# Kernel optimization log

Hardware: AMD Instinct MI355X
Metric: run time of the kernel (lower is better)

The kernel has to match this reference:

```python
import jax, jax.numpy as jnp
import numpy as np

B, T, IN, H = 1024, 128, 5, 100  # batch, seq_len, input_size, hidden_size


def setup_inputs() -> dict:
    key = jax.random.key(0)
    ks = jax.random.split(key, 20)
    bound = 1.0 / np.sqrt(H)  # PyTorch LSTM init: U(-1/sqrt(H), 1/sqrt(H))

    def u(k, shape):
        return jax.random.uniform(k, shape, jnp.float32, -bound, bound)

    inp = {"x": jax.random.normal(ks[0], (B, T, IN), jnp.float32)}
    i = 1
    for layer, din in [(0, IN), (1, 2 * H)]:
        for d in ("f", "b"):
            inp[f"w_ih_l{layer}{d}"] = u(ks[i], (4 * H, din)); i += 1
            inp[f"w_hh_l{layer}{d}"] = u(ks[i], (4 * H, H)); i += 1
            inp[f"b_ih_l{layer}{d}"] = u(ks[i], (4 * H,)); i += 1
            inp[f"b_hh_l{layer}{d}"] = u(ks[i], (4 * H,)); i += 1
    inp["fc_w"] = u(ks[17], (3, 2 * H))
    inp["fc_b"] = u(ks[18], (3,))
    return inp


def _run_dir(x, w_ih, w_hh, b_ih, b_hh, reverse):
    """One LSTM direction. x: [B,T,D] -> hidden seq [B,T,H]. PyTorch gate order i,f,g,o."""
    xT = jnp.swapaxes(x, 0, 1)  # [T,B,D]
    # precompute input contribution for all timesteps: [T,B,4H]
    xg = jnp.einsum('tbd,gd->tbg', xT, w_ih) + b_ih + b_hh

    def step(carry, g_in):
        h, c = carry
        g = g_in + h @ w_hh.T  # [B,4H]
        i, f, gg, o = jnp.split(g, 4, axis=-1)
        c = jax.nn.sigmoid(f) * c + jax.nn.sigmoid(i) * jnp.tanh(gg)
        h = jax.nn.sigmoid(o) * jnp.tanh(c)
        return (h, c), h

    b = x.shape[0]
    init = (jnp.zeros((b, H), x.dtype), jnp.zeros((b, H), x.dtype))
    _, hs = jax.lax.scan(step, init, xg, reverse=reverse)  # hs[t] aligned with time t
    return jnp.swapaxes(hs, 0, 1)  # [B,T,H]


def reference(x,
              w_ih_l0f, w_hh_l0f, b_ih_l0f, b_hh_l0f,
              w_ih_l0b, w_hh_l0b, b_ih_l0b, b_hh_l0b,
              w_ih_l1f, w_hh_l1f, b_ih_l1f, b_hh_l1f,
              w_ih_l1b, w_hh_l1b, b_ih_l1b, b_hh_l1b,
              fc_w, fc_b):
    # Layer 0 (bidirectional): [B,T,2H]
    h0 = jnp.concatenate([
        _run_dir(x, w_ih_l0f, w_hh_l0f, b_ih_l0f, b_hh_l0f, False),
        _run_dir(x, w_ih_l0b, w_hh_l0b, b_ih_l0b, b_hh_l0b, True),
    ], axis=-1)
    # (inter-layer dropout p=0.2 is identity in eval mode)
    # Layer 1 (bidirectional): [B,T,2H]
    h1 = jnp.concatenate([
        _run_dir(h0, w_ih_l1f, w_hh_l1f, b_ih_l1f, b_hh_l1f, False),
        _run_dir(h0, w_ih_l1b, w_hh_l1b, b_ih_l1b, b_hh_l1b, True),
    ], axis=-1)
    last = h1[:, -1, :]  # [B,2H]
    # (dropout p=0.5 is identity in eval mode)
    logits = last @ fc_w.T + fc_b  # [B,3]
    return jax.nn.softmax(logits, axis=1)
```

## Files before the change

kernel.cpp:

```cpp
#include <hip/hip_runtime.h>
#include <hip/hip_fp16.h>


typedef __attribute__((ext_vector_type(8))) short bf16x8;
typedef __attribute__((ext_vector_type(4))) float f32x4;

constexpr int Bsz = 1024, Tt = 128, IN_ = 5, H = 100, G = 400, D1 = 200;
constexpr int NP = 512;
constexpr int NT = 25;
constexpr int MB = 8;
constexpr int MB1 = 4;

__device__ __forceinline__ float sigm(float x)   { return 1.f / (1.f + __expf(-x)); }
__device__ __forceinline__ float tanhf_(float x) { return 1.f - 2.f / (__expf(2.f * x) + 1.f); }
__device__ __forceinline__ unsigned short f2bf(float f) {
  unsigned u = __float_as_uint(f);
  u += 0x7fff + ((u >> 16) & 1);
  return (unsigned short)(u >> 16);
}
__device__ __forceinline__ float partner8(float v) {
  return __uint_as_float(
      (unsigned)__builtin_amdgcn_ds_swizzle((int)__float_as_uint(v), 0x17));
}
__device__ __forceinline__ float partner4(float v) {
  return __uint_as_float(
      (unsigned)__builtin_amdgcn_ds_swizzle((int)__float_as_uint(v), 0x13));
}

__device__ __forceinline__ void pack_body(
    const float* wA, int KA, const float* wB, int KB, int kbo,
    const float* b1, const float* b2, int bias_k,
    unsigned short* dst, int Kg, int idx) {
  if (idx >= Kg * NP * 8) return;
  int jj = idx & 7, rest = idx >> 3;
  int np_ = rest % NP, g = rest / NP;
  int j = np_ >> 2, gate = np_ & 3;
  int k = g * 8 + jj;
  float v = 0.f;
  if (j < H) {
    int n = gate * H + j;
    if (k < KA) v = wA[n * KA + k];
    else if (KB > 0 && k >= kbo && k < kbo + KB) v = wB[n * KB + (k - kbo)];
    else if (k == bias_k) v = b1[n] + b2[n];
  }
  dst[idx] = f2bf(v);
}

__global__ void pack_all(
    const float* __restrict__ w_hh_l0f, const float* __restrict__ w_ih_l0f,
    const float* __restrict__ b_ih_l0f, const float* __restrict__ b_hh_l0f,
    const float* __restrict__ w_hh_l0b, const float* __restrict__ w_ih_l0b,
    const float* __restrict__ b_ih_l0b, const float* __restrict__ b_hh_l0b,
    const float* __restrict__ w_hh_l1f, const float* __restrict__ b_ih_l1f,
    const float* __restrict__ b_hh_l1f,
    const float* __restrict__ w_ih_l1f, const float* __restrict__ w_ih_l1b,
    const float* __restrict__ b_ih_l1b, const float* __restrict__ b_hh_l1b,
    unsigned short* __restrict__ pk0f, unsigned short* __restrict__ pk0b,
    unsigned short* __restrict__ pkhh, unsigned short* __restrict__ pkxg,
    unsigned short* __restrict__ pk1b) {
  int idx = blockIdx.x * 256 + threadIdx.x;
  switch (blockIdx.y) {
    case 0: pack_body(w_hh_l0f, 100, w_ih_l0f, 5, 100, b_ih_l0f, b_hh_l0f, 105, pk0f, 16, idx); break;
    case 1: pack_body(w_hh_l0b, 100, w_ih_l0b, 5, 100, b_ih_l0b, b_hh_l0b, 105, pk0b, 16, idx); break;
    case 2: pack_body(w_hh_l1f, 100, nullptr, 0, 0, b_ih_l1f, b_hh_l1f, -1, pkhh, 16, idx); break;
    case 3: pack_body(w_ih_l1f, 200, nullptr, 0, 0, b_ih_l1f, b_hh_l1f, 200, pkxg, 28, idx); break;
    default: pack_body(w_ih_l1b, 200, nullptr, 0, 0, b_ih_l1b, b_hh_l1b, 200, pk1b, 28, idx);
  }
}

__global__ __launch_bounds__(1024, 1) void lstm_l0(
    const float* __restrict__ x,
    const unsigned short* __restrict__ pk_f, const unsigned short* __restrict__ pk_b,
    unsigned short* __restrict__ h0fT, unsigned short* __restrict__ h0bT) {
  __shared__ __align__(16) short A_s[2][16][16][8];

  const int tid = threadIdx.x;
  const int lane = tid & 63, w = tid >> 6;
  const int q = lane >> 4, l16 = lane & 15;
  const int b0 = blockIdx.x * MB;
  const int dir = blockIdx.y;
  const unsigned short* pk = dir ? pk_b : pk_f;
  unsigned short* hT = dir ? h0bT : h0fT;

  for (int i = tid; i < 2 * 16 * 16 * 8; i += 1024) ((short*)A_s)[i] = 0;

  const int mtA = w, mtB = w + 16;
  const bool bvalid = (mtB < NT);
  bf16x8 wfA[4], wfB[4];
#pragma unroll
  for (int kt = 0; kt < 4; ++kt) {
    wfA[kt] = *(const bf16x8*)(pk + ((size_t)(kt * 4 + q) * NP + mtA * 16 + l16) * 8);
    wfB[kt] = *(const bf16x8*)(pk + ((size_t)(kt * 4 + q) * NP + mtB * 16 + l16) * 8);
  }
  float c = 0.f;
  const bool up = (l16 >= 8);
  const int mm = l16 & 7;
  const int j = (up ? mtB : mtA) * 4 + q;
  const bool valid = up ? bvalid : true;
  const int xm = tid / IN_, xe = tid - xm * IN_;
  const int sm = tid / 25, sj = (tid - (tid / 25) * 25) * 4;
  const float* xp = x + ((size_t)(b0 + xm) * Tt + (dir ? Tt - 2 : 1)) * IN_ + xe;
  const int xstride = dir ? -IN_ : IN_;
  unsigned short* hp =
      hT + ((size_t)(dir ? Tt - 1 : 0) * Bsz + b0 + sm) * H + sj;
  const int hstride = dir ? -(Bsz * H) : (Bsz * H);
  __syncthreads();
  if (tid < 16) {
    A_s[0][13][tid][1] = (short)f2bf(1.f);
    A_s[1][13][tid][1] = (short)f2bf(1.f);
  }
  if (tid < MB * IN_) {
    int t0 = dir ? (Tt - 1) : 0;
    int k = 100 + xe;
    A_s[0][k >> 3][xm][k & 7] =
        (short)f2bf(x[((size_t)(b0 + xm) * Tt + t0) * IN_ + xe]);
  }
  __syncthreads();

  int p = 0;
  for (int step = 0; step < Tt; ++step) {
    if (step > 0 && tid < 200) {
      uint2 hv = *(const uint2*)&A_s[p][sj >> 3][sm][sj & 7];
      *(uint2*)hp = hv;
      hp += hstride;
    }
    float xn = 0.f;
    const bool do_x = (tid < MB * IN_) && (step < Tt - 1);
    if (do_x) { xn = *xp; xp += xstride; }
    bf16x8 hfrag[4];
#pragma unroll
    for (int kt = 0; kt < 4; ++kt) hfrag[kt] = *(const bf16x8*)A_s[p][kt * 4 + q][l16];
    f32x4 accA = (f32x4){0.f, 0.f, 0.f, 0.f};
    f32x4 accB = (f32x4){0.f, 0.f, 0.f, 0.f};
#pragma unroll
    for (int kt = 0; kt < 4; ++kt)
      accA = __builtin_amdgcn_mfma_f32_16x16x32_bf16(wfA[kt], hfrag[kt], accA, 0, 0, 0);
    if (bvalid) {
#pragma unroll
      for (int kt = 0; kt < 4; ++kt)
        accB = __builtin_amdgcn_mfma_f32_16x16x32_bf16(wfB[kt], hfrag[kt], accB, 0, 0, 0);
    }
    float pb0 = partner8(accB[0]), pb1 = partner8(accB[1]);
    float pb2 = partner8(accB[2]), pb3 = partner8(accB[3]);
    float g0 = up ? pb0 : accA[0];
    float g1 = up ? pb1 : accA[1];
    float g2 = up ? pb2 : accA[2];
    float g3 = up ? pb3 : accA[3];
    float cc = sigm(g1) * c + sigm(g0) * tanhf_(g2);
    c = cc;
    float h = sigm(g3) * tanhf_(cc);
    if (valid) A_s[1 - p][j >> 3][mm][j & 7] = (short)f2bf(h);
    if (do_x) {
      int k = 100 + xe;
      A_s[1 - p][k >> 3][xm][k & 7] = (short)f2bf(xn);
    }
    __syncthreads();
    p ^= 1;
  }
  if (tid < 200) *(uint2*)hp = *(const uint2*)&A_s[p][sj >> 3][sm][sj & 7];
}

__global__ __launch_bounds__(1024, 1) void gemm_xg(
    const unsigned short* __restrict__ h0fT, const unsigned short* __restrict__ h0bT,
    const unsigned short* __restrict__ pkw, __half* __restrict__ xg) {
  __shared__ __align__(16) short B_s[28][64][8];
  const int tid = threadIdx.x;
  const int lane = tid & 63, w = tid >> 6;
  const int q = lane >> 4, l16 = lane & 15;
  const int r0 = blockIdx.x * 64;
  const size_t base = (size_t)r0 * H;

  for (int i = tid; i < 3 * 64 * 8; i += 1024) {
    int jj = i & 7, gl = i >> 9;
    ((short*)&B_s[25][0][0])[i] = (short)((gl == 0 && jj == 0) ? f2bf(1.f) : 0);
  }
  for (int idx = tid; idx < 1600; idx += 1024) {
    int m = idx / 25, j0 = (idx - (idx / 25) * 25) * 4;
    *(uint2*)&B_s[j0 >> 3][m][j0 & 7] = *(const uint2*)(h0fT + base + m * H + j0);
    int k = 100 + j0;
    *(uint2*)&B_s[k >> 3][m][k & 7] = *(const uint2*)(h0bT + base + m * H + j0);
  }

  const int mtA = w, mtB = w + 16;
  const bool bvalid = (mtB < NT);
  bf16x8 wfA[7], wfB[7];
#pragma unroll
  for (int kt = 0; kt < 7; ++kt) {
    wfA[kt] = *(const bf16x8*)(pkw + ((size_t)(kt * 4 + q) * NP + mtA * 16 + l16) * 8);
    wfB[kt] = *(const bf16x8*)(pkw + ((size_t)(kt * 4 + q) * NP + mtB * 16 + l16) * 8);
  }
  const int jA = mtA * 4 + q, jB = mtB * 4 + q;
  __syncthreads();

#pragma unroll
  for (int rg = 0; rg < 4; ++rg) {
    f32x4 accA = (f32x4){0.f, 0.f, 0.f, 0.f};
    f32x4 accB = (f32x4){0.f, 0.f, 0.f, 0.f};
#pragma unroll
    for (int kt = 0; kt < 7; ++kt) {
      bf16x8 hf = *(const bf16x8*)B_s[kt * 4 + q][rg * 16 + l16];
      accA = __builtin_amdgcn_mfma_f32_16x16x32_bf16(wfA[kt], hf, accA, 0, 0, 0);
      if (bvalid)
        accB = __builtin_amdgcn_mfma_f32_16x16x32_bf16(wfB[kt], hf, accB, 0, 0, 0);
    }
    const size_t row = (size_t)(r0 + rg * 16 + l16);
    {
      __half2 h01 = __floats2half2_rn(accA[0], accA[1]);
      __half2 h23 = __floats2half2_rn(accA[2], accA[3]);
      uint2 st; *(__half2*)&st.x = h01; *(__half2*)&st.y = h23;
      *(uint2*)(xg + row * G + 4 * jA) = st;
    }
    if (bvalid) {
      __half2 h01 = __floats2half2_rn(accB[0], accB[1]);
      __half2 h23 = __floats2half2_rn(accB[2], accB[3]);
      uint2 st; *(__half2*)&st.x = h01; *(__half2*)&st.y = h23;
      *(uint2*)(xg + row * G + 4 * jB) = st;
    }
  }
}

__global__ __launch_bounds__(1024, 1) void lstm_l1(
    const unsigned short* __restrict__ h0fT, const unsigned short* __restrict__ h0bT,
    const unsigned short* __restrict__ pk_hh, const unsigned short* __restrict__ pk1b,
    const __half* __restrict__ xg,
    const float* __restrict__ fc_w, const float* __restrict__ fc_b,
    float* __restrict__ out) {
  __shared__ __align__(16) short A_s[2][16][16][8];
  __shared__ __align__(16) short A2_s[28][16][8];
  __shared__ float hf_s[MB1][H];
  __shared__ float hb_s[MB1][H];
  __shared__ float fcw_s[3 * D1];
  __shared__ float fcb_s[3];
  __shared__ float logit_s[MB1][3];

  const int tid = threadIdx.x;
  const int lane = tid & 63, w = tid >> 6;
  const int q = lane >> 4, l16 = lane & 15;
  const int b0 = blockIdx.x * MB1;
  const uint2* xg2 = (const uint2*)xg;

  for (int i = tid; i < 2 * 16 * 16 * 8; i += 1024) ((short*)A_s)[i] = 0;
  for (int i = tid; i < 25 * 16 * 8; i += 1024) ((short*)A2_s)[i] = 0;
  for (int i = tid; i < 3 * 16 * 8; i += 1024) {
    int jj = i & 7, gl = i >> 7;
    ((short*)&A2_s[25][0][0])[i] = (short)((gl == 0 && jj == 0) ? f2bf(1.f) : 0);
  }
  for (int i = tid; i < 3 * D1; i += 1024) fcw_s[i] = fc_w[i];
  if (tid < 3) fcb_s[tid] = fc_b[tid];

  const bool busy = (w < 7);
  const int m = l16 & 3, g16 = l16 >> 2;
  const int myMt = w * 4 + g16;
  const int jme = myMt * 4 + q;
  const bool evalid = busy && (myMt < NT);
  int mts[4]; bool tv[4];
  bf16x8 wf[4][4];
  if (busy) {
#pragma unroll
    for (int i = 0; i < 4; ++i) {
      int mt = w * 4 + i; mts[i] = mt; tv[i] = (mt < NT);
#pragma unroll
      for (int kt = 0; kt < 4; ++kt)
        wf[i][kt] = *(const bf16x8*)(pk_hh + ((size_t)(kt * 4 + q) * NP + mt * 16 + l16) * 8);
    }
  }
  float c = 0.f;
  const uint2* xgp = xg2 + (size_t)(b0 + m) * 100 + jme;
  uint2 xgCur = {0, 0};
  if (busy) { xgCur = *xgp; xgp += Bsz * 100; }
  __syncthreads();

  int p = 0;
  for (int t = 0; t < Tt; ++t) {
    if (busy) {
      uint2 xgNxt = xgCur;
      if (t < Tt - 1) { xgNxt = *xgp; xgp += Bsz * 100; }
      bf16x8 hfrag[4];
#pragma unroll
      for (int kt = 0; kt < 4; ++kt) hfrag[kt] = *(const bf16x8*)A_s[p][kt * 4 + q][l16];
      f32x4 acc[4];
#pragma unroll
      for (int i = 0; i < 4; ++i) {
        acc[i] = (f32x4){0.f, 0.f, 0.f, 0.f};
        if (!tv[i]) continue;
#pragma unroll
        for (int kt = 0; kt < 4; ++kt)
          acc[i] = __builtin_amdgcn_mfma_f32_16x16x32_bf16(wf[i][kt], hfrag[kt], acc[i], 0, 0, 0);
      }
      float2 x01 = __half22float2(*(const __half2*)&xgCur.x);
      float2 x23 = __half22float2(*(const __half2*)&xgCur.y);
      float xr[4] = {x01.x, x01.y, x23.x, x23.y};
      float gr[4];
#pragma unroll
      for (int r = 0; r < 4; ++r) {
        float v0 = partner4(acc[0][r]);
        float v1 = partner4(acc[1][r]);
        float v2 = partner4(acc[2][r]);
        float v3 = partner4(acc[3][r]);
        float lo = (g16 & 1) ? v1 : v0;
        float hi = (g16 & 1) ? v3 : v2;
        gr[r] = ((g16 & 2) ? hi : lo) + xr[r];
      }
      float cc = sigm(gr[1]) * c + sigm(gr[0]) * tanhf_(gr[2]);
      c = cc;
      float h = sigm(gr[3]) * tanhf_(cc);
      if (evalid) {
        A_s[1 - p][jme >> 3][m][jme & 7] = (short)f2bf(h);
        if (t == Tt - 1) hf_s[m][jme] = h;
      }
      xgCur = xgNxt;
    }
    __syncthreads();
    p ^= 1;
  }

  {
    const size_t base = ((size_t)(Tt - 1) * Bsz + b0) * H;
    if (tid < 100) {
      int m2 = tid / 25, j0 = (tid - (tid / 25) * 25) * 4;
      *(uint2*)&A2_s[j0 >> 3][m2][j0 & 7] = *(const uint2*)(h0fT + base + m2 * H + j0);
      int k = 100 + j0;
      *(uint2*)&A2_s[k >> 3][m2][k & 7] = *(const uint2*)(h0bT + base + m2 * H + j0);
    }
  }
  __syncthreads();
  if (busy) {
    f32x4 acc[4];
#pragma unroll
    for (int i = 0; i < 4; ++i) acc[i] = (f32x4){0.f, 0.f, 0.f, 0.f};
#pragma unroll
    for (int kt = 0; kt < 7; ++kt) {
      bf16x8 hf = *(const bf16x8*)A2_s[kt * 4 + q][l16];
#pragma unroll
      for (int i = 0; i < 4; ++i) {
        if (!tv[i]) continue;
        bf16x8 wfb = *(const bf16x8*)(pk1b + ((size_t)(kt * 4 + q) * NP + mts[i] * 16 + l16) * 8);
        acc[i] = __builtin_amdgcn_mfma_f32_16x16x32_bf16(wfb, hf, acc[i], 0, 0, 0);
      }
    }
    float gr[4];
#pragma unroll
    for (int r = 0; r < 4; ++r) {
      float v0 = partner4(acc[0][r]);
      float v1 = partner4(acc[1][r]);
      float v2 = partner4(acc[2][r]);
      float v3 = partner4(acc[3][r]);
      float lo = (g16 & 1) ? v1 : v0;
      float hi = (g16 & 1) ? v3 : v2;
      gr[r] = (g16 & 2) ? hi : lo;
    }
    float cc = sigm(gr[0]) * tanhf_(gr[2]);
    if (evalid) hb_s[m][jme] = sigm(gr[3]) * tanhf_(cc);
  }
  __syncthreads();

  if (tid < MB1 * 3) {
    int mr = tid / 3, cls = tid - mr * 3;
    float s = fcb_s[cls];
    for (int jj = 0; jj < H; ++jj) s += fcw_s[cls * D1 + jj] * hf_s[mr][jj];
    for (int jj = 0; jj < H; ++jj) s += fcw_s[cls * D1 + H + jj] * hb_s[mr][jj];
    logit_s[mr][cls] = s;
  }
  __syncthreads();
  if (tid < MB1) {
    float a = logit_s[tid][0], b = logit_s[tid][1], cc = logit_s[tid][2];
    float mx = fmaxf(a, fmaxf(b, cc));
    float e0 = __expf(a - mx), e1 = __expf(b - mx), e2 = __expf(cc - mx);
    float inv = 1.f / (e0 + e1 + e2);
    out[(b0 + tid) * 3 + 0] = e0 * inv;
    out[(b0 + tid) * 3 + 1] = e1 * inv;
    out[(b0 + tid) * 3 + 2] = e2 * inv;
  }
}

extern "C" void kernel_launch(void* const* d_in, const int* in_sizes, int n_in,
                              void* d_out, int out_size, void* d_ws, size_t ws_size,
                              hipStream_t stream) {
  const float* x        = (const float*)d_in[0];
  const float* w_ih_l0f = (const float*)d_in[1];
  const float* w_hh_l0f = (const float*)d_in[2];
  const float* b_ih_l0f = (const float*)d_in[3];
  const float* b_hh_l0f = (const float*)d_in[4];
  const float* w_ih_l0b = (const float*)d_in[5];
  const float* w_hh_l0b = (const float*)d_in[6];
  const float* b_ih_l0b = (const float*)d_in[7];
  const float* b_hh_l0b = (const float*)d_in[8];
  const float* w_ih_l1f = (const float*)d_in[9];
  const float* w_hh_l1f = (const float*)d_in[10];
  const float* b_ih_l1f = (const float*)d_in[11];
  const float* b_hh_l1f = (const float*)d_in[12];
  const float* w_ih_l1b = (const float*)d_in[13];
  const float* b_ih_l1b = (const float*)d_in[15];
  const float* b_hh_l1b = (const float*)d_in[16];
  const float* fc_w     = (const float*)d_in[17];
  const float* fc_b     = (const float*)d_in[18];

  unsigned short* h0fT = (unsigned short*)d_ws;
  unsigned short* h0bT = h0fT + (size_t)Tt * Bsz * H;
  __half* xgT          = (__half*)(h0bT + (size_t)Tt * Bsz * H);
  unsigned short* pk0f = (unsigned short*)(xgT + (size_t)Tt * Bsz * G);
  unsigned short* pk0b = pk0f + 16 * NP * 8;
  unsigned short* pkhh = pk0b + 16 * NP * 8;
  unsigned short* pkxg = pkhh + 16 * NP * 8;
  unsigned short* pk1b = pkxg + 28 * NP * 8;

  pack_all<<<dim3(448, 5), 256, 0, stream>>>(
      w_hh_l0f, w_ih_l0f, b_ih_l0f, b_hh_l0f,
      w_hh_l0b, w_ih_l0b, b_ih_l0b, b_hh_l0b,
      w_hh_l1f, b_ih_l1f, b_hh_l1f,
      w_ih_l1f, w_ih_l1b, b_ih_l1b, b_hh_l1b,
      pk0f, pk0b, pkhh, pkxg, pk1b);

  lstm_l0<<<dim3(Bsz / MB, 2), 1024, 0, stream>>>(x, pk0f, pk0b, h0fT, h0bT);
  gemm_xg<<<(Bsz * Tt) / 64, 1024, 0, stream>>>(h0fT, h0bT, pkxg, xgT);
  lstm_l1<<<Bsz / MB1, 1024, 0, stream>>>(h0fT, h0bT, pkhh, pk1b, xgT,
                                          fc_w, fc_b, (float*)d_out);
}
```

Measured before the change: 383.4 us.

## Halve per-block batch in both LSTM kernels and use 512-thread blocks with more occupancy

Cuts the batch rows per block (8 to 4 in layer 0, 4 to 2 in layer 1) and shrinks blocks to 512 threads with launch bounds allowing 4 blocks per CU. Layer 0 is rebuilt so each of 7 busy waves handles four gate tiles, with a partner4 swizzle replacing the old two-tile split. Layer 1 switches to a partner2 swizzle for the narrower batch. The aim is more blocks in flight so the serial recurrence latency is hidden across more CUs. In exchange, more MFMA work is spent on padded batch columns and each block reloads the weights.

```diff
diff --git a/kernel.cpp b/kernel.cpp
--- a/kernel.cpp
+++ b/kernel.cpp
@@ -8,8 +8,8 @@
 constexpr int Bsz = 1024, Tt = 128, IN_ = 5, H = 100, G = 400, D1 = 200;
 constexpr int NP = 512;
 constexpr int NT = 25;
-constexpr int MB = 8;
-constexpr int MB1 = 4;
+constexpr int MB = 4;
+constexpr int MB1 = 2;
 
 __device__ __forceinline__ float sigm(float x)   { return 1.f / (1.f + __expf(-x)); }
 __device__ __forceinline__ float tanhf_(float x) { return 1.f - 2.f / (__expf(2.f * x) + 1.f); }
@@ -18,13 +18,13 @@
   u += 0x7fff + ((u >> 16) & 1);
   return (unsigned short)(u >> 16);
 }
-__device__ __forceinline__ float partner8(float v) {
-  return __uint_as_float(
-      (unsigned)__builtin_amdgcn_ds_swizzle((int)__float_as_uint(v), 0x17));
-}
 __device__ __forceinline__ float partner4(float v) {
   return __uint_as_float(
       (unsigned)__builtin_amdgcn_ds_swizzle((int)__float_as_uint(v), 0x13));
+}
+__device__ __forceinline__ float partner2(float v) {
+  return __uint_as_float(
+      (unsigned)__builtin_amdgcn_ds_swizzle((int)__float_as_uint(v), 0x11));
 }
 
 __device__ __forceinline__ void pack_body(
@@ -68,7 +68,7 @@
   }
 }
 
-__global__ __launch_bounds__(1024, 1) void lstm_l0(
+__global__ __launch_bounds__(512, 4) void lstm_l0(
     const float* __restrict__ x,
     const unsigned short* __restrict__ pk_f, const unsigned short* __restrict__ pk_b,
     unsigned short* __restrict__ h0fT, unsigned short* __restrict__ h0bT) {
@@ -82,22 +82,29 @@
   const unsigned short* pk = dir ? pk_b : pk_f;
   unsigned short* hT = dir ? h0bT : h0fT;
 
-  for (int i = tid; i < 2 * 16 * 16 * 8; i += 1024) ((short*)A_s)[i] = 0;
-
-  const int mtA = w, mtB = w + 16;
-  const bool bvalid = (mtB < NT);
-  bf16x8 wfA[4], wfB[4];
-#pragma unroll
-  for (int kt = 0; kt < 4; ++kt) {
-    wfA[kt] = *(const bf16x8*)(pk + ((size_t)(kt * 4 + q) * NP + mtA * 16 + l16) * 8);
-    wfB[kt] = *(const bf16x8*)(pk + ((size_t)(kt * 4 + q) * NP + mtB * 16 + l16) * 8);
+  for (int i = tid; i < 2 * 16 * 16 * 8; i += 512) ((short*)A_s)[i] = 0;
+
+  const bool busy = (w < 7);
+  const int m = l16 & 3, g16 = l16 >> 2;
+  const int myMt = w * 4 + g16;
+  const int jme = myMt * 4 + q;
+  const bool evalid = busy && (myMt < NT);
+  bool tv[4];
+  bf16x8 wf[4][4];
+  if (busy) {
+#pragma unroll
+    for (int i = 0; i < 4; ++i) {
+      int mt = w * 4 + i; tv[i] = (mt < NT);
+#pragma unroll
+      for (int kt = 0; kt < 4; ++kt)
+        wf[i][kt] = *(const bf16x8*)(pk + ((size_t)(kt * 4 + q) * NP + mt * 16 + l16) * 8);
+    }
   }
   float c = 0.f;
-  const bool up = (l16 >= 8);
-  const int mm = l16 & 7;
-  const int j = (up ? mtB : mtA) * 4 + q;
-  const bool valid = up ? bvalid : true;
-  const int xm = tid / IN_, xe = tid - xm * IN_;
+  const int xt = tid - 448;
+  const bool xl = (xt >= 0 && xt < MB * IN_);
+  const int xm = xl ? xt / IN_ : 0;
+  const int xe = xl ? xt - xm * IN_ : 0;
   const int sm = tid / 25, sj = (tid - (tid / 25) * 25) * 4;
   const float* xp = x + ((size_t)(b0 + xm) * Tt + (dir ? Tt - 2 : 1)) * IN_ + xe;
   const int xstride = dir ? -IN_ : IN_;
@@ -111,45 +118,51 @@
   }
   if (tid < MB * IN_) {
     int t0 = dir ? (Tt - 1) : 0;
-    int k = 100 + xe;
-    A_s[0][k >> 3][xm][k & 7] =
-        (short)f2bf(x[((size_t)(b0 + xm) * Tt + t0) * IN_ + xe]);
+    int m0 = tid / IN_, e0 = tid - m0 * IN_;
+    int k = 100 + e0;
+    A_s[0][k >> 3][m0][k & 7] =
+        (short)f2bf(x[((size_t)(b0 + m0) * Tt + t0) * IN_ + e0]);
   }
   __syncthreads();
 
   int p = 0;
   for (int step = 0; step < Tt; ++step) {
-    if (step > 0 && tid < 200) {
-      uint2 hv = *(const uint2*)&A_s[p][sj >> 3][sm][sj & 7];
-      *(uint2*)hp = hv;
+    if (step > 0 && tid < 100) {
+      *(uint2*)hp = *(const uint2*)&A_s[p][sj >> 3][sm][sj & 7];
       hp += hstride;
     }
     float xn = 0.f;
-    const bool do_x = (tid < MB * IN_) && (step < Tt - 1);
+    const bool do_x = xl && (step < Tt - 1);
     if (do_x) { xn = *xp; xp += xstride; }
-    bf16x8 hfrag[4];
-#pragma unroll
-    for (int kt = 0; kt < 4; ++kt) hfrag[kt] = *(const bf16x8*)A_s[p][kt * 4 + q][l16];
-    f32x4 accA = (f32x4){0.f, 0.f, 0.f, 0.f};
-    f32x4 accB = (f32x4){0.f, 0.f, 0.f, 0.f};
-#pragma unroll
-    for (int kt = 0; kt < 4; ++kt)
-      accA = __builtin_amdgcn_mfma_f32_16x16x32_bf16(wfA[kt], hfrag[kt], accA, 0, 0, 0);
-    if (bvalid) {
-#pragma unroll
-      for (int kt = 0; kt < 4; ++kt)
-        accB = __builtin_amdgcn_mfma_f32_16x16x32_bf16(wfB[kt], hfrag[kt], accB, 0, 0, 0);
-    }
-    float pb0 = partner8(accB[0]), pb1 = partner8(accB[1]);
-    float pb2 = partner8(accB[2]), pb3 = partner8(accB[3]);
-    float g0 = up ? pb0 : accA[0];
-    float g1 = up ? pb1 : accA[1];
-    float g2 = up ? pb2 : accA[2];
-    float g3 = up ? pb3 : accA[3];
-    float cc = sigm(g1) * c + sigm(g0) * tanhf_(g2);
-    c = cc;
-    float h = sigm(g3) * tanhf_(cc);
-    if (valid) A_s[1 - p][j >> 3][mm][j & 7] = (short)f2bf(h);
+    if (busy) {
+      bf16x8 hfrag[4];
+#pragma unroll
+      for (int kt = 0; kt < 4; ++kt) hfrag[kt] = *(const bf16x8*)A_s[p][kt * 4 + q][l16];
+      f32x4 acc[4];
+#pragma unroll
+      for (int i = 0; i < 4; ++i) {
+        acc[i] = (f32x4){0.f, 0.f, 0.f, 0.f};
+        if (!tv[i]) continue;
+#pragma unroll
+        for (int kt = 0; kt < 4; ++kt)
+          acc[i] = __builtin_amdgcn_mfma_f32_16x16x32_bf16(wf[i][kt], hfrag[kt], acc[i], 0, 0, 0);
+      }
+      float gr[4];
+#pragma unroll
+      for (int r = 0; r < 4; ++r) {
+        float v0 = partner4(acc[0][r]);
+        float v1 = partner4(acc[1][r]);
+        float v2 = partner4(acc[2][r]);
+        float v3 = partner4(acc[3][r]);
+        float lo = (g16 & 1) ? v1 : v0;
+        float hi = (g16 & 1) ? v3 : v2;
+        gr[r] = (g16 & 2) ? hi : lo;
+      }
+      float cc = sigm(gr[1]) * c + sigm(gr[0]) * tanhf_(gr[2]);
+      c = cc;
+      float h = sigm(gr[3]) * tanhf_(cc);
+      if (evalid) A_s[1 - p][jme >> 3][m][jme & 7] = (short)f2bf(h);
+    }
     if (do_x) {
       int k = 100 + xe;
       A_s[1 - p][k >> 3][xm][k & 7] = (short)f2bf(xn);
@@ -157,7 +170,7 @@
     __syncthreads();
     p ^= 1;
   }
-  if (tid < 200) *(uint2*)hp = *(const uint2*)&A_s[p][sj >> 3][sm][sj & 7];
+  if (tid < 100) *(uint2*)hp = *(const uint2*)&A_s[p][sj >> 3][sm][sj & 7];
 }
 
 __global__ __launch_bounds__(1024, 1) void gemm_xg(
@@ -219,7 +232,7 @@
   }
 }
 
-__global__ __launch_bounds__(1024, 1) void lstm_l1(
+__global__ __launch_bounds__(512, 4) void lstm_l1(
     const unsigned short* __restrict__ h0fT, const unsigned short* __restrict__ h0bT,
     const unsigned short* __restrict__ pk_hh, const unsigned short* __restrict__ pk1b,
     const __half* __restrict__ xg,
@@ -239,26 +252,26 @@
   const int b0 = blockIdx.x * MB1;
   const uint2* xg2 = (const uint2*)xg;
 
-  for (int i = tid; i < 2 * 16 * 16 * 8; i += 1024) ((short*)A_s)[i] = 0;
-  for (int i = tid; i < 25 * 16 * 8; i += 1024) ((short*)A2_s)[i] = 0;
-  for (int i = tid; i < 3 * 16 * 8; i += 1024) {
+  for (int i = tid; i < 2 * 16 * 16 * 8; i += 512) ((short*)A_s)[i] = 0;
+  for (int i = tid; i < 25 * 16 * 8; i += 512) ((short*)A2_s)[i] = 0;
+  for (int i = tid; i < 3 * 16 * 8; i += 512) {
     int jj = i & 7, gl = i >> 7;
     ((short*)&A2_s[25][0][0])[i] = (short)((gl == 0 && jj == 0) ? f2bf(1.f) : 0);
   }
-  for (int i = tid; i < 3 * D1; i += 1024) fcw_s[i] = fc_w[i];
+  for (int i = tid; i < 3 * D1; i += 512) fcw_s[i] = fc_w[i];
   if (tid < 3) fcb_s[tid] = fc_b[tid];
 
   const bool busy = (w < 7);
-  const int m = l16 & 3, g16 = l16 >> 2;
+  const int m = l16 & 1, g16 = (l16 >> 1) & 3;
   const int myMt = w * 4 + g16;
   const int jme = myMt * 4 + q;
-  const bool evalid = busy && (myMt < NT);
-  int mts[4]; bool tv[4];
+  const bool evalid = busy && (myMt < NT) && (l16 < 8);
+  bool tv[4];
   bf16x8 wf[4][4];
   if (busy) {
 #pragma unroll
     for (int i = 0; i < 4; ++i) {
-      int mt = w * 4 + i; mts[i] = mt; tv[i] = (mt < NT);
+      int mt = w * 4 + i; tv[i] = (mt < NT);
 #pragma unroll
       for (int kt = 0; kt < 4; ++kt)
         wf[i][kt] = *(const bf16x8*)(pk_hh + ((size_t)(kt * 4 + q) * NP + mt * 16 + l16) * 8);
@@ -293,10 +306,10 @@
       float gr[4];
 #pragma unroll
       for (int r = 0; r < 4; ++r) {
-        float v0 = partner4(acc[0][r]);
-        float v1 = partner4(acc[1][r]);
-        float v2 = partner4(acc[2][r]);
-        float v3 = partner4(acc[3][r]);
+        float v0 = partner2(acc[0][r]);
+        float v1 = partner2(acc[1][r]);
+        float v2 = partner2(acc[2][r]);
+        float v3 = partner2(acc[3][r]);
         float lo = (g16 & 1) ? v1 : v0;
         float hi = (g16 & 1) ? v3 : v2;
         gr[r] = ((g16 & 2) ? hi : lo) + xr[r];
@@ -316,7 +329,7 @@
 
   {
     const size_t base = ((size_t)(Tt - 1) * Bsz + b0) * H;
-    if (tid < 100) {
+    if (tid < MB1 * 25) {
       int m2 = tid / 25, j0 = (tid - (tid / 25) * 25) * 4;
       *(uint2*)&A2_s[j0 >> 3][m2][j0 & 7] = *(const uint2*)(h0fT + base + m2 * H + j0);
       int k = 100 + j0;
@@ -334,17 +347,18 @@
 #pragma unroll
       for (int i = 0; i < 4; ++i) {
         if (!tv[i]) continue;
-        bf16x8 wfb = *(const bf16x8*)(pk1b + ((size_t)(kt * 4 + q) * NP + mts[i] * 16 + l16) * 8);
+        int mt = w * 4 + i;
+        bf16x8 wfb = *(const bf16x8*)(pk1b + ((size_t)(kt * 4 + q) * NP + mt * 16 + l16) * 8);
         acc[i] = __builtin_amdgcn_mfma_f32_16x16x32_bf16(wfb, hf, acc[i], 0, 0, 0);
       }
     }
     float gr[4];
 #pragma unroll
     for (int r = 0; r < 4; ++r) {
-      float v0 = partner4(acc[0][r]);
-      float v1 = partner4(acc[1][r]);
-      float v2 = partner4(acc[2][r]);
-      float v3 = partner4(acc[3][r]);
+      float v0 = partner2(acc[0][r]);
+      float v1 = partner2(acc[1][r]);
+      float v2 = partner2(acc[2][r]);
+      float v3 = partner2(acc[3][r]);
       float lo = (g16 & 1) ? v1 : v0;
       float hi = (g16 & 1) ? v3 : v2;
       gr[r] = (g16 & 2) ? hi : lo;
@@ -411,8 +425,8 @@
       w_ih_l1f, w_ih_l1b, b_ih_l1b, b_hh_l1b,
       pk0f, pk0b, pkhh, pkxg, pk1b);
 
-  lstm_l0<<<dim3(Bsz / MB, 2), 1024, 0, stream>>>(x, pk0f, pk0b, h0fT, h0bT);
+  lstm_l0<<<dim3(Bsz / MB, 2), 512, 0, stream>>>(x, pk0f, pk0b, h0fT, h0bT);
   gemm_xg<<<(Bsz * Tt) / 64, 1024, 0, stream>>>(h0fT, h0bT, pkxg, xgT);
-  lstm_l1<<<Bsz / MB1, 1024, 0, stream>>>(h0fT, h0bT, pkhh, pk1b, xgT,
-                                          fc_w, fc_b, (float*)d_out);
-}
+  lstm_l1<<<Bsz / MB1, 512, 0, stream>>>(h0fT, h0bT, pkhh, pk1b, xgT,
+                                         fc_w, fc_b, (float*)d_out);
+}
```

Result: slower. 473.2 us (+23.4%).
